# Performance work log

Measured on AMD Instinct MI355X. Metric: run time of the kernel, lower is better.

## Reference

```python
import jax, jax.numpy as jnp
import numpy as np

B, S, H = 2, 2048, 1024
I = 1024          # moe_intermediate_size
E = 8             # n_routed_experts
K = 2             # num_experts_per_tok
SCALE = 1.0       # routed_scaling_factor


def setup_inputs() -> dict:
    key = jax.random.key(0)
    ks = jax.random.split(key, 8)
    sd = 1.0 / np.sqrt(H)
    si = 1.0 / np.sqrt(I)
    return {
        "hidden_states": jax.random.normal(ks[0], (B, S, H), jnp.float32),
        "router_w": jax.random.uniform(ks[1], (E, H), jnp.float32, -sd, sd),
        # shared expert (n_shared_experts = 1); weights stored [in, out]
        "shared_gate": jax.random.uniform(ks[2], (H, I), jnp.float32, -sd, sd),
        "shared_up": jax.random.uniform(ks[3], (H, I), jnp.float32, -sd, sd),
        "shared_down": jax.random.uniform(ks[4], (I, H), jnp.float32, -si, si),
        # routed experts, stacked [E, in, out]
        "experts_gate": jax.random.uniform(ks[5], (E, H, I), jnp.float32, -sd, sd),
        "experts_up": jax.random.uniform(ks[6], (E, H, I), jnp.float32, -sd, sd),
        "experts_down": jax.random.uniform(ks[7], (E, I, H), jnp.float32, -si, si),
    }


def reference(hidden_states, router_w, shared_gate, shared_up, shared_down,
              experts_gate, experts_up, experts_down):
    residual = hidden_states
    x = hidden_states.reshape(-1, H)                      # [T, H], T = B*S

    # shared expert (SwiGLU-ish: sigmoid(gate) * up)
    sg = x @ shared_gate
    su = x @ shared_up
    shared_out = (jax.nn.sigmoid(sg) * su) @ shared_down  # [T, H]

    # router: softmax over experts, greedy top-k
    logits = x @ router_w.T                               # [T, E]
    scores = jax.nn.softmax(logits.astype(jnp.float32), axis=-1)
    topk_w, topk_idx = jax.lax.top_k(scores, K)           # [T, K]
    topk_w = topk_w * SCALE

    # dense compute of ALL experts on all tokens (faithful to reference)
    g = jnp.einsum('th,ehi->tei', x, experts_gate)        # [T, E, I]
    u = jnp.einsum('th,ehi->tei', x, experts_up)
    hid = jax.nn.sigmoid(g) * u
    expert_outputs = jnp.einsum('tei,eih->teh', hid, experts_down)  # [T, E, H]

    # gather top-k expert outputs and combine
    selected = jnp.take_along_axis(expert_outputs, topk_idx[:, :, None], axis=1)  # [T, K, H]
    routed_out = (selected * topk_w[:, :, None]).sum(axis=1)                      # [T, H]

    out = residual + (shared_out + routed_out).reshape(B, S, H)
    return out
```

## Files before the change

kernel.cpp:

```cpp
#include <hip/hip_runtime.h>
#include <hip/hip_bf16.h>

#define T_TOK 4096
#define HDIM 1024
#define IDIM 1024
#define EDIM 8
#define HID_SHARED_BASE 8320

typedef __attribute__((ext_vector_type(8))) short bf16x8;
typedef __attribute__((ext_vector_type(4))) float f32x4;

static __device__ __forceinline__ unsigned short f2bf(float f) {
  union { float f; unsigned int u; } v; v.f = f;
  unsigned int u = v.u;
  unsigned int r = u + 0x7FFFu + ((u >> 16) & 1u);
  return (unsigned short)(r >> 16);
}

#define GLD16(g, l) __builtin_amdgcn_global_load_lds( \
    (const __attribute__((address_space(1))) void*)(g), \
    (__attribute__((address_space(3))) void*)(l), 16, 0, 0)

__global__ __launch_bounds__(256) void convert_x(const float4* __restrict__ x4,
                                                 ushort4* __restrict__ xb4,
                                                 float4* __restrict__ out4) {
  int i = blockIdx.x * 256 + threadIdx.x;
  float4 v = x4[i];
  out4[i] = v;
  ushort4 o;
  o.x = f2bf(v.x); o.y = f2bf(v.y); o.z = f2bf(v.z); o.w = f2bf(v.w);
  xb4[i] = o;
}

__global__ void zero_cnt(int* __restrict__ cnt) {
  if (threadIdx.x < 16) cnt[threadIdx.x] = 0;
}

struct SrcPtrs { const float* p[6]; };

__global__ __launch_bounds__(256) void transpose_all(SrcPtrs S,
                                                     unsigned short* __restrict__ dstBase) {
  __shared__ unsigned short t[32][36];
  const int z = blockIdx.z;
  const float* src; int dz;
  if (z == 0)      { src = S.p[0];                              dz = 8;  }
  else if (z == 1) { src = S.p[1];                              dz = 17; }
  else if (z == 2) { src = S.p[2];                              dz = 26; }
  else if (z < 11) { src = S.p[3] + (size_t)(z - 3)  * 1048576; dz = z - 3; }
  else if (z < 19) { src = S.p[4] + (size_t)(z - 11) * 1048576; dz = 9 + (z - 11); }
  else             { src = S.p[5] + (size_t)(z - 19) * 1048576; dz = 18 + (z - 19); }
  unsigned short* dst = dstBase + (size_t)dz * 1048576;

  const int r0 = blockIdx.y * 32;
  const int c0 = blockIdx.x * 32;
  const int tid = threadIdx.x;
  const int rr = tid >> 3;
  const int cc = (tid & 7) * 4;
  const float4 v = *(const float4*)&src[(size_t)(r0 + rr) * 1024 + c0 + cc];
  t[rr][cc + 0] = f2bf(v.x); t[rr][cc + 1] = f2bf(v.y);
  t[rr][cc + 2] = f2bf(v.z); t[rr][cc + 3] = f2bf(v.w);
  __syncthreads();
  ushort4 o;
  o.x = t[cc + 0][rr]; o.y = t[cc + 1][rr]; o.z = t[cc + 2][rr]; o.w = t[cc + 3][rr];
  *(ushort4*)&dst[(size_t)(c0 + rr) * 1024 + r0 + cc] = o;
}

__global__ __launch_bounds__(256) void router2(
    const float* __restrict__ x, const float* __restrict__ rw,
    int* __restrict__ cnt, int* __restrict__ list, float* __restrict__ wgt) {
  __shared__ float rwT[1024 * 8];
  const int tid = threadIdx.x;
#pragma unroll
  for (int c = 0; c < 4; c++) {
    const int h = c * 256 + tid;
    float v[8];
#pragma unroll
    for (int e = 0; e < EDIM; e++) v[e] = rw[e * 1024 + h];
    *(float4*)&rwT[h * 8]     = make_float4(v[0], v[1], v[2], v[3]);
    *(float4*)&rwT[h * 8 + 4] = make_float4(v[4], v[5], v[6], v[7]);
  }
  __syncthreads();

  const int tt = tid >> 4;
  const int pp = tid & 15;
  const int t = blockIdx.x * 16 + tt;
  const float* xr = x + (size_t)t * HDIM;

  float a[EDIM];
#pragma unroll
  for (int e = 0; e < EDIM; e++) a[e] = 0.f;

#pragma unroll 8
  for (int i = 0; i < 64; i++) {
    const int h = pp + 16 * i;
    const float xs = xr[h];
    const float4 r0 = *(const float4*)&rwT[h * 8];
    const float4 r1 = *(const float4*)&rwT[h * 8 + 4];
    a[0] += xs * r0.x; a[1] += xs * r0.y; a[2] += xs * r0.z; a[3] += xs * r0.w;
    a[4] += xs * r1.x; a[5] += xs * r1.y; a[6] += xs * r1.z; a[7] += xs * r1.w;
  }
#pragma unroll
  for (int s = 1; s < 16; s <<= 1) {
#pragma unroll
    for (int e = 0; e < EDIM; e++) a[e] += __shfl_xor(a[e], s, 16);
  }
  if (pp == 0) {
    float m = a[0];
#pragma unroll
    for (int e = 1; e < EDIM; e++) m = fmaxf(m, a[e]);
    float p[EDIM]; float s = 0.f;
#pragma unroll
    for (int e = 0; e < EDIM; e++) { p[e] = expf(a[e] - m); s += p[e]; }
    float inv = 1.f / s;
    int e1 = 0; float b1 = p[0];
#pragma unroll
    for (int e = 1; e < EDIM; e++) if (p[e] > b1) { b1 = p[e]; e1 = e; }
    int e2 = -1; float b2 = -1.f;
#pragma unroll
    for (int e = 0; e < EDIM; e++) if (e != e1 && p[e] > b2) { b2 = p[e]; e2 = e; }
    int pos1 = atomicAdd(&cnt[e1], 1);
    list[e1 * T_TOK + pos1] = t; wgt[e1 * T_TOK + pos1] = b1 * inv;
    int pos2 = atomicAdd(&cnt[e2], 1);
    list[e2 * T_TOK + pos2] = t; wgt[e2 * T_TOK + pos2] = b2 * inv;
  }
}

__global__ __launch_bounds__(256) void gateup_f(
    const unsigned short* __restrict__ xb,
    const unsigned short* __restrict__ gateT,
    const unsigned short* __restrict__ upT,
    unsigned short* __restrict__ hid,
    const int* __restrict__ cnt, const int* __restrict__ list) {
  __shared__ unsigned short Al[2][128 * 32];
  __shared__ unsigned short Bg[2][64 * 32];
  __shared__ unsigned short Bu[2][64 * 32];

  const int tid = threadIdx.x;
  const int lane = tid & 63;
  const int w = tid >> 6;
  const int wm = w >> 1, wn = w & 1;
  const int z = blockIdx.z;
  const int m0 = blockIdx.y * 128;
  const int n0 = blockIdx.x * 64;

  int count, hidbase;
  if (z < EDIM) {
    count = cnt[z];
    if (m0 >= count) return;
    int off = 0;
#pragma unroll
    for (int i = 0; i < EDIM; i++) off += (i < z) ? cnt[i] : 0;
    hidbase = off;
  } else {
    count = T_TOK;
    hidbase = HID_SHARED_BASE;
  }
  const unsigned short* wg = gateT + (size_t)z * HDIM * IDIM;
  const unsigned short* wu = upT   + (size_t)z * HDIM * IDIM;

  const unsigned short* gA[2];
#pragma unroll
  for (int j = 0; j < 2; j++) {
    const int s = w * 128 + j * 64 + lane;
    const int row = s >> 2;
    const int g = (s & 3) ^ ((row + (row >> 2)) & 3);
    int tok;
    if (z < EDIM) {
      int p = m0 + row; if (p >= count) p = count - 1;
      tok = list[z * T_TOK + p];
    } else tok = m0 + row;
    gA[j] = xb + (size_t)tok * HDIM + g * 8;
  }
  const int sB = w * 64 + lane;
  const int rowB = sB >> 2;
  const int gB = (sB & 3) ^ ((rowB + (rowB >> 2)) & 3);
  const unsigned short* gGp = wg + (size_t)(n0 + rowB) * HDIM + gB * 8;
  const unsigned short* gUp = wu + (size_t)(n0 + rowB) * HDIM + gB * 8;

  f32x4 accg[4][2], accu[4][2];
  const f32x4 z4 = {0.f, 0.f, 0.f, 0.f};
#pragma unroll
  for (int i = 0; i < 4; i++)
#pragma unroll
    for (int j = 0; j < 2; j++) { accg[i][j] = z4; accu[i][j] = z4; }

  const int q = lane >> 4;
  const int r16 = lane & 15;
  const int ch = (q ^ ((r16 + (r16 >> 2)) & 3)) * 8;

  auto stage = [&](int k0, int b) {
    GLD16(gA[0] + k0, &Al[b][(w * 128) * 8]);
    GLD16(gA[1] + k0, &Al[b][(w * 128 + 64) * 8]);
    GLD16(gGp + k0, &Bg[b][(w * 64) * 8]);
    GLD16(gUp + k0, &Bu[b][(w * 64) * 8]);
  };
  auto compute = [&](int b) {
    bf16x8 af[4], bg2[2], bu2[2];
#pragma unroll
    for (int i = 0; i < 4; i++)
      af[i] = *(const bf16x8*)&Al[b][(wm * 64 + i * 16 + r16) * 32 + ch];
#pragma unroll
    for (int j = 0; j < 2; j++) {
      bg2[j] = *(const bf16x8*)&Bg[b][(wn * 32 + j * 16 + r16) * 32 + ch];
      bu2[j] = *(const bf16x8*)&Bu[b][(wn * 32 + j * 16 + r16) * 32 + ch];
    }
#pragma unroll
    for (int i = 0; i < 4; i++)
#pragma unroll
      for (int j = 0; j < 2; j++) {
        accg[i][j] = __builtin_amdgcn_mfma_f32_16x16x32_bf16(af[i], bg2[j], accg[i][j], 0, 0, 0);
        accu[i][j] = __builtin_amdgcn_mfma_f32_16x16x32_bf16(af[i], bu2[j], accu[i][j], 0, 0, 0);
      }
  };

  stage(0, 0);
#pragma unroll 1
  for (int p = 0; p < 16; p++) {
    __syncthreads();
    stage((2 * p + 1) * 32, 1);
    compute(0);
    __syncthreads();
    if (p < 15) stage((2 * p + 2) * 32, 0);
    compute(1);
  }

#pragma unroll
  for (int i = 0; i < 4; i++) {
#pragma unroll
    for (int j = 0; j < 2; j++) {
      const int col = n0 + wn * 32 + j * 16 + r16;
#pragma unroll
      for (int r = 0; r < 4; r++) {
        int pos = m0 + wm * 64 + i * 16 + q * 4 + r;
        if (pos < count) {
          float g = accg[i][j][r], u = accu[i][j][r];
          float h = u / (1.f + __expf(-g));
          hid[(size_t)(hidbase + pos) * IDIM + col] = f2bf(h);
        }
      }
    }
  }
}

__global__ __launch_bounds__(256) void down_f(
    const unsigned short* __restrict__ hid,
    const unsigned short* __restrict__ downT,
    float* __restrict__ out,
    const int* __restrict__ cnt, const int* __restrict__ list,
    const float* __restrict__ wgt) {
  __shared__ unsigned short Al[2][128 * 32];
  __shared__ unsigned short Bl[2][128 * 32];

  const int tid = threadIdx.x;
  const int lane = tid & 63;
  const int w = tid >> 6;
  const int wm = w >> 1, wn = w & 1;
  const int z = blockIdx.z;
  const int m0 = blockIdx.y * 128;
  const int n0 = blockIdx.x * 128;

  int count, abase;
  if (z < EDIM) {
    count = cnt[z];
    if (m0 >= count) return;
    int off = 0;
#pragma unroll
    for (int i = 0; i < EDIM; i++) off += (i < z) ? cnt[i] : 0;
    abase = off;
  } else {
    count = T_TOK;
    abase = HID_SHARED_BASE;
  }
  const unsigned short* wd = downT + (size_t)z * IDIM * HDIM;

  const unsigned short *gA[2], *gBp[2];
#pragma unroll
  for (int j = 0; j < 2; j++) {
    const int s = w * 128 + j * 64 + lane;
    const int row = s >> 2;
    const int g = (s & 3) ^ ((row + (row >> 2)) & 3);
    gA[j]  = hid + (size_t)(abase + m0 + row) * IDIM + g * 8;
    gBp[j] = wd + (size_t)(n0 + row) * IDIM + g * 8;
  }

  f32x4 acc[4][4];
  const f32x4 z4 = {0.f, 0.f, 0.f, 0.f};
#pragma unroll
  for (int i = 0; i < 4; i++)
#pragma unroll
    for (int j = 0; j < 4; j++) acc[i][j] = z4;

  const int q = lane >> 4;
  const int r16 = lane & 15;
  const int ch = (q ^ ((r16 + (r16 >> 2)) & 3)) * 8;

  auto stage = [&](int k0, int b) {
    GLD16(gA[0] + k0,  &Al[b][(w * 128) * 8]);
    GLD16(gA[1] + k0,  &Al[b][(w * 128 + 64) * 8]);
    GLD16(gBp[0] + k0, &Bl[b][(w * 128) * 8]);
    GLD16(gBp[1] + k0, &Bl[b][(w * 128 + 64) * 8]);
  };
  auto compute = [&](int b) {
    bf16x8 af[4], bf4[4];
#pragma unroll
    for (int i = 0; i < 4; i++)
      af[i] = *(const bf16x8*)&Al[b][(wm * 64 + i * 16 + r16) * 32 + ch];
#pragma unroll
    for (int j = 0; j < 4; j++)
      bf4[j] = *(const bf16x8*)&Bl[b][(wn * 64 + j * 16 + r16) * 32 + ch];
#pragma unroll
    for (int i = 0; i < 4; i++)
#pragma unroll
      for (int j = 0; j < 4; j++)
        acc[i][j] = __builtin_amdgcn_mfma_f32_16x16x32_bf16(af[i], bf4[j], acc[i][j], 0, 0, 0);
  };

  stage(0, 0);
#pragma unroll 1
  for (int p = 0; p < 16; p++) {
    __syncthreads();
    stage((2 * p + 1) * 32, 1);
    compute(0);
    __syncthreads();
    if (p < 15) stage((2 * p + 2) * 32, 0);
    compute(1);
  }

#pragma unroll
  for (int i = 0; i < 4; i++) {
    int toks[4]; float ws4[4];
#pragma unroll
    for (int r = 0; r < 4; r++) {
      int pos = m0 + wm * 64 + i * 16 + q * 4 + r;
      if (z < EDIM) {
        bool ok = pos < count;
        toks[r] = ok ? list[z * T_TOK + pos] : -1;
        ws4[r] = ok ? wgt[z * T_TOK + pos] : 0.f;
      } else {
        toks[r] = pos; ws4[r] = 1.f;
      }
    }
#pragma unroll
    for (int j = 0; j < 4; j++) {
      const int col = n0 + wn * 64 + j * 16 + r16;
#pragma unroll
      for (int r = 0; r < 4; r++) {
        if (toks[r] >= 0)
          atomicAdd(&out[(size_t)toks[r] * HDIM + col], ws4[r] * acc[i][j][r]);
      }
    }
  }
}

extern "C" void kernel_launch(void* const* d_in, const int* in_sizes, int n_in,
                              void* d_out, int out_size, void* d_ws, size_t ws_size,
                              hipStream_t stream) {
  const float* x  = (const float*)d_in[0];
  const float* rw = (const float*)d_in[1];
  const float* sg = (const float*)d_in[2];
  const float* su = (const float*)d_in[3];
  const float* sd = (const float*)d_in[4];
  const float* eg = (const float*)d_in[5];
  const float* eu = (const float*)d_in[6];
  const float* ed = (const float*)d_in[7];
  float* out = (float*)d_out;

  char* ws = (char*)d_ws;
  unsigned short* xb  = (unsigned short*)ws;
  unsigned short* hid = xb + (size_t)T_TOK * HDIM;
  int*   cnt  = (int*)(hid + (size_t)(HID_SHARED_BASE + T_TOK) * IDIM);
  int*   list = cnt + 16;
  float* wgt  = (float*)(list + EDIM * T_TOK);
  unsigned short* wT    = (unsigned short*)(wgt + EDIM * T_TOK);
  unsigned short* gateT = wT;
  unsigned short* upT   = wT + (size_t)9 * 1048576;
  unsigned short* downT = wT + (size_t)18 * 1048576;

  zero_cnt<<<1, 64, 0, stream>>>(cnt);
  convert_x<<<(T_TOK * HDIM) / 1024, 256, 0, stream>>>(
      (const float4*)x, (ushort4*)xb, (float4*)out);
  router2<<<T_TOK / 16, 256, 0, stream>>>(x, rw, cnt, list, wgt);

  SrcPtrs S; S.p[0] = sg; S.p[1] = su; S.p[2] = sd; S.p[3] = eg; S.p[4] = eu; S.p[5] = ed;
  transpose_all<<<dim3(32, 32, 27), 256, 0, stream>>>(S, wT);

  gateup_f<<<dim3(IDIM / 64, 32, 9), 256, 0, stream>>>(xb, gateT, upT, hid, cnt, list);
  down_f<<<dim3(HDIM / 128, 32, 9), 256, 0, stream>>>(hid, downT, out, cnt, list, wgt);
}
```

Measured before the change: 386.8 us.

## Triple-buffer GEMM K-loop with vmcnt waits and widen weight transpose tiles

The gate/up and down GEMM kernels move from a double-buffered loop with two __syncthreads per iteration to a triple-buffered pipeline. Each step waits on outstanding global-to-LDS loads with an explicit s_waitcnt vmcnt and then issues a single barrier, which keeps two stages in flight. The weight transpose kernel also switches to 64x64 tiles with an XOR-swizzled LDS layout and 16-byte stores. The extra buffer raises LDS use and could lower occupancy. The hardcoded vmcnt(4) assumes each stage issues exactly 4 loads per thread, and gets ordering wrong if that does not hold.

```diff
diff --git a/kernel.cpp b/kernel.cpp
--- a/kernel.cpp
+++ b/kernel.cpp
@@ -40,7 +40,7 @@
 
 __global__ __launch_bounds__(256) void transpose_all(SrcPtrs S,
                                                      unsigned short* __restrict__ dstBase) {
-  __shared__ unsigned short t[32][36];
+  __shared__ unsigned short t[64][72];
   const int z = blockIdx.z;
   const float* src; int dz;
   if (z == 0)      { src = S.p[0];                              dz = 8;  }
@@ -51,18 +51,34 @@
   else             { src = S.p[5] + (size_t)(z - 19) * 1048576; dz = 18 + (z - 19); }
   unsigned short* dst = dstBase + (size_t)dz * 1048576;
 
-  const int r0 = blockIdx.y * 32;
-  const int c0 = blockIdx.x * 32;
+  const int r0 = blockIdx.y * 64;
+  const int c0 = blockIdx.x * 64;
   const int tid = threadIdx.x;
-  const int rr = tid >> 3;
-  const int cc = (tid & 7) * 4;
-  const float4 v = *(const float4*)&src[(size_t)(r0 + rr) * 1024 + c0 + cc];
-  t[rr][cc + 0] = f2bf(v.x); t[rr][cc + 1] = f2bf(v.y);
-  t[rr][cc + 2] = f2bf(v.z); t[rr][cc + 3] = f2bf(v.w);
+
+  const int rr = tid >> 4;
+  const int c4 = (tid & 15) * 4;
+#pragma unroll
+  for (int ph = 0; ph < 4; ph++) {
+    const int r = rr + ph * 16;
+    const float4 v = *(const float4*)&src[(size_t)(r0 + r) * 1024 + c0 + c4];
+    const int cs = c4 ^ (4 * (r >> 3));
+    t[r][cs + 0] = f2bf(v.x); t[r][cs + 1] = f2bf(v.y);
+    t[r][cs + 2] = f2bf(v.z); t[r][cs + 3] = f2bf(v.w);
+  }
   __syncthreads();
-  ushort4 o;
-  o.x = t[cc + 0][rr]; o.y = t[cc + 1][rr]; o.z = t[cc + 2][rr]; o.w = t[cc + 3][rr];
-  *(ushort4*)&dst[(size_t)(c0 + rr) * 1024 + r0 + cc] = o;
+
+  const int n = tid >> 3;
+  const int k8 = (tid & 7) * 8;
+  const int m = k8 >> 3;
+#pragma unroll
+  for (int ph = 0; ph < 2; ph++) {
+    const int nn = n + ph * 32;
+    const int ns = nn ^ (4 * m);
+    unsigned short v[8];
+#pragma unroll
+    for (int j = 0; j < 8; j++) v[j] = t[k8 + j][ns];
+    *(bf16x8*)&dst[(size_t)(c0 + nn) * 1024 + r0 + k8] = *(const bf16x8*)v;
+  }
 }
 
 __global__ __launch_bounds__(256) void router2(
@@ -131,9 +147,9 @@
     const unsigned short* __restrict__ upT,
     unsigned short* __restrict__ hid,
     const int* __restrict__ cnt, const int* __restrict__ list) {
-  __shared__ unsigned short Al[2][128 * 32];
-  __shared__ unsigned short Bg[2][64 * 32];
-  __shared__ unsigned short Bu[2][64 * 32];
+  __shared__ unsigned short Al[3][128 * 32];
+  __shared__ unsigned short Bg[3][64 * 32];
+  __shared__ unsigned short Bu[3][64 * 32];
 
   const int tid = threadIdx.x;
   const int lane = tid & 63;
@@ -214,14 +230,17 @@
   };
 
   stage(0, 0);
+  stage(32, 1);
 #pragma unroll 1
-  for (int p = 0; p < 16; p++) {
-    __syncthreads();
-    stage((2 * p + 1) * 32, 1);
-    compute(0);
-    __syncthreads();
-    if (p < 15) stage((2 * p + 2) * 32, 0);
-    compute(1);
+  for (int p = 0; p < 32; p++) {
+    if (p < 30) {
+      asm volatile("s_waitcnt vmcnt(4)" ::: "memory");
+    } else {
+      asm volatile("s_waitcnt vmcnt(0)" ::: "memory");
+    }
+    __builtin_amdgcn_s_barrier();
+    if (p + 2 < 32) stage((p + 2) * 32, (p + 2) % 3);
+    compute(p % 3);
   }
 
 #pragma unroll
@@ -248,8 +267,8 @@
     float* __restrict__ out,
     const int* __restrict__ cnt, const int* __restrict__ list,
     const float* __restrict__ wgt) {
-  __shared__ unsigned short Al[2][128 * 32];
-  __shared__ unsigned short Bl[2][128 * 32];
+  __shared__ unsigned short Al[3][128 * 32];
+  __shared__ unsigned short Bl[3][128 * 32];
 
   const int tid = threadIdx.x;
   const int lane = tid & 63;
@@ -316,14 +335,17 @@
   };
 
   stage(0, 0);
+  stage(32, 1);
 #pragma unroll 1
-  for (int p = 0; p < 16; p++) {
-    __syncthreads();
-    stage((2 * p + 1) * 32, 1);
-    compute(0);
-    __syncthreads();
-    if (p < 15) stage((2 * p + 2) * 32, 0);
-    compute(1);
+  for (int p = 0; p < 32; p++) {
+    if (p < 30) {
+      asm volatile("s_waitcnt vmcnt(4)" ::: "memory");
+    } else {
+      asm volatile("s_waitcnt vmcnt(0)" ::: "memory");
+    }
+    __builtin_amdgcn_s_barrier();
+    if (p + 2 < 32) stage((p + 2) * 32, (p + 2) % 3);
+    compute(p % 3);
   }
 
 #pragma unroll
@@ -382,7 +404,7 @@
   router2<<<T_TOK / 16, 256, 0, stream>>>(x, rw, cnt, list, wgt);
 
   SrcPtrs S; S.p[0] = sg; S.p[1] = su; S.p[2] = sd; S.p[3] = eg; S.p[4] = eu; S.p[5] = ed;
-  transpose_all<<<dim3(32, 32, 27), 256, 0, stream>>>(S, wT);
+  transpose_all<<<dim3(16, 16, 27), 256, 0, stream>>>(S, wT);
 
   gateup_f<<<dim3(IDIM / 64, 32, 9), 256, 0, stream>>>(xb, gateT, upT, hid, cnt, list);
   down_f<<<dim3(HDIM / 128, 32, 9), 256, 0, stream>>>(hid, downT, out, cnt, list, wgt);
```

Result: faster. 378.5 us (-2.1%).
